# Performance work log

Hardware: AMD Instinct MI355X
Metric: run time of the kernel (lower is better)

Reference implementation:

```python
import jax, jax.numpy as jnp
import numpy as np
import math

D_MODEL = 512
N_HEADS = 8
D_K = D_MODEL // N_HEADS
BS, N_EDGES, N_NODES = 4, 1024, 4096


def setup_inputs() -> dict:
    key = jax.random.key(0)
    ks = jax.random.split(key, 12)
    s = 1.0 / math.sqrt(D_MODEL)
    return {
        "queries": jax.random.normal(ks[0], (BS, N_EDGES, D_MODEL), jnp.float32),
        "keys": jax.random.normal(ks[1], (BS, N_NODES, D_MODEL), jnp.float32),
        "incidence_matrix": jax.random.randint(ks[2], (BS, N_EDGES, N_NODES), 0, 2, jnp.int32),
        "Wq": jax.random.normal(ks[3], (D_MODEL, D_MODEL), jnp.float32) * s,
        "bq": jax.random.normal(ks[4], (D_MODEL,), jnp.float32) * s,
        "Wk": jax.random.normal(ks[5], (D_MODEL, D_MODEL), jnp.float32) * s,
        "bk": jax.random.normal(ks[6], (D_MODEL,), jnp.float32) * s,
        "Wv": jax.random.normal(ks[7], (D_MODEL, D_MODEL), jnp.float32) * s,
        "bv": jax.random.normal(ks[8], (D_MODEL,), jnp.float32) * s,
        "Wo": jax.random.normal(ks[9], (D_MODEL, D_MODEL), jnp.float32) * s,
        "bo": jax.random.normal(ks[10], (D_MODEL,), jnp.float32) * s,
    }


def reference(queries, keys, incidence_matrix, Wq, bq, Wk, bk, Wv, bv, Wo, bo):
    bs, E, _ = queries.shape
    N = keys.shape[1]
    # QKV projections (torch Linear: x @ W.T + b), split heads -> (bs, H, len, d_k)
    Q = (queries @ Wq.T + bq).reshape(bs, E, N_HEADS, D_K).transpose(0, 2, 1, 3)
    K = (keys @ Wk.T + bk).reshape(bs, N, N_HEADS, D_K).transpose(0, 2, 1, 3)
    V = (keys @ Wv.T + bv).reshape(bs, N, N_HEADS, D_K).transpose(0, 2, 1, 3)
    # scores: (bs, H, E, N)
    scores = jnp.einsum("bhed,bhnd->bhen", Q, K) / math.sqrt(D_K)
    mask = (incidence_matrix == 0)[:, None, :, :]  # (bs, 1, E, N)
    scores = jnp.where(mask, jnp.float32(-1e9), scores)
    attn = jax.nn.softmax(scores, axis=-1)
    # dropout is identity in eval mode
    out = jnp.einsum("bhen,bhnd->bhed", attn, V)  # (bs, H, E, d_k)
    out = out.transpose(0, 2, 1, 3).reshape(bs, E, D_MODEL)
    return out @ Wo.T + bo
```

## Files before the change

kernel.cpp:

```cpp
#include <hip/hip_runtime.h>

#define DMODEL 512
#define NHEADS 8
#define DK 64
#define BSZ 4
#define NE 1024
#define NNODE 4096

typedef __attribute__((ext_vector_type(8))) __bf16 bf16x8;
typedef __attribute__((ext_vector_type(4))) float f32x4;
typedef __attribute__((ext_vector_type(8))) unsigned short u16x8;
typedef __attribute__((ext_vector_type(4))) unsigned short u16x4;

static __device__ __forceinline__ unsigned short f2bf(float f) {
    union { float f; unsigned int u; } v; v.f = f;
    unsigned int u = v.u;
    return (unsigned short)((u + 0x7FFFu + ((u >> 16) & 1u)) >> 16);
}

static __device__ __forceinline__ unsigned cvtpk(float lo, float hi) {
    unsigned r;
    asm("v_cvt_pk_bf16_f32 %0, %1, %2" : "=v"(r) : "v"(lo), "v"(hi));
    return r;
}

static __device__ __forceinline__ float exp2v(float x) {
    float r;
    asm("v_exp_f32 %0, %1" : "=v"(r) : "v"(x));
    return r;
}

static __device__ __forceinline__ bf16x8 ldb8(const unsigned short* p) {
    return *reinterpret_cast<const bf16x8*>(p);
}

static __device__ __forceinline__ void gload16(const unsigned short* g,
                                               unsigned short* l) {
    __builtin_amdgcn_global_load_lds(
        (const __attribute__((address_space(1))) unsigned int*)g,
        (__attribute__((address_space(3))) unsigned int*)l, 16, 0, 0);
}

__global__ __launch_bounds__(256) void conv_all(
    const float4* __restrict__ q, const float4* __restrict__ k,
    const float4* __restrict__ wq, const float4* __restrict__ wk,
    const float4* __restrict__ wv, const float4* __restrict__ wo,
    u16x8* __restrict__ qb, u16x8* __restrict__ kb, u16x8* __restrict__ wb) {
    int i = blockIdx.x * 256 + threadIdx.x;
    const float4* s;
    u16x8* d;
    int j;
    if (i < 262144) {
        s = q; d = qb; j = i;
    } else if (i < 1310720) {
        s = k; d = kb; j = i - 262144;
    } else {
        int t = i - 1310720;
        int sel = t >> 15;
        s = sel == 0 ? wq : sel == 1 ? wk : sel == 2 ? wv : wo;
        d = wb + ((size_t)sel << 15);
        j = t & 32767;
    }
    float4 x = s[2 * j];
    float4 y = s[2 * j + 1];
    unsigned u0 = cvtpk(x.x, x.y), u1 = cvtpk(x.z, x.w);
    unsigned u2 = cvtpk(y.x, y.y), u3 = cvtpk(y.z, y.w);
    u16x8 o;
    o[0] = (unsigned short)u0; o[1] = (unsigned short)(u0 >> 16);
    o[2] = (unsigned short)u1; o[3] = (unsigned short)(u1 >> 16);
    o[4] = (unsigned short)u2; o[5] = (unsigned short)(u2 >> 16);
    o[6] = (unsigned short)u3; o[7] = (unsigned short)(u3 >> 16);
    d[j] = o;
}

__global__ __launch_bounds__(256) void maskpack(const int* __restrict__ inc,
                                                unsigned long long* __restrict__ mb) {
    int wid = blockIdx.x * 4 + (threadIdx.x >> 6);
    int lane = threadIdx.x & 63;
#pragma unroll
    for (int j = 0; j < 8; ++j) {
        int g = wid * 8 + j;
        int v = inc[(size_t)g * 64 + lane];
        unsigned long long m = __ballot(v != 0);
        if (lane == 0) mb[g] = m;
    }
}

template <int MODE>
__global__ __launch_bounds__(256) void gemm128(const unsigned short* __restrict__ A,
                                               const unsigned short* __restrict__ W,
                                               const float* __restrict__ bias,
                                               void* __restrict__ Cout, float oscale) {
    int w = threadIdx.x >> 6, l = threadIdx.x & 63;
    int lr = l & 15, lh = l >> 4;
    int wm = w >> 1, wn = w & 1;
    int m0 = blockIdx.x * 128, n0 = blockIdx.y * 128;

    __shared__ unsigned short Ast[2][128][64];
    __shared__ unsigned short Bst[2][128][64];

    int srow = w * 32 + (l >> 3);
    int scu = l & 7;

    auto stage = [&](int bf, int k0) {
#pragma unroll
        for (int ii = 0; ii < 4; ++ii) {
            int row = srow + ii * 8;
            int cu = scu ^ (row & 7);
            gload16(A + (size_t)(m0 + row) * DMODEL + k0 + cu * 8,
                    &Ast[bf][w * 32 + ii * 8][0]);
            gload16(W + (size_t)(n0 + row) * DMODEL + k0 + cu * 8,
                    &Bst[bf][w * 32 + ii * 8][0]);
        }
    };

    f32x4 acc[4][4] = {};

    stage(0, 0);
    __syncthreads();

    int bf = 0;
    for (int t = 0; t < 8; ++t) {
        if (t < 7) stage(bf ^ 1, (t + 1) * 64);
#pragma unroll
        for (int half = 0; half < 2; ++half) {
            bf16x8 af[4], bfr[4];
#pragma unroll
            for (int mf = 0; mf < 4; ++mf)
                af[mf] = ldb8(&Ast[bf][wm * 64 + mf * 16 + lr]
                                  [((half * 4 + lh) ^ (lr & 7)) * 8]);
#pragma unroll
            for (int nf = 0; nf < 4; ++nf)
                bfr[nf] = ldb8(&Bst[bf][wn * 64 + nf * 16 + lr]
                                   [((half * 4 + lh) ^ (lr & 7)) * 8]);
#pragma unroll
            for (int mf = 0; mf < 4; ++mf)
#pragma unroll
                for (int nf = 0; nf < 4; ++nf)
                    acc[mf][nf] = __builtin_amdgcn_mfma_f32_16x16x32_bf16(
                        af[mf], bfr[nf], acc[mf][nf], 0, 0, 0);
        }
        __syncthreads();
        bf ^= 1;
    }

    if constexpr (MODE == 0) {
        unsigned short* C = (unsigned short*)Cout;
#pragma unroll
        for (int nf = 0; nf < 4; ++nf) {
            int ncol = n0 + wn * 64 + nf * 16 + lr;
            float bv = bias[ncol];
#pragma unroll
            for (int mf = 0; mf < 4; ++mf)
#pragma unroll
                for (int r = 0; r < 4; ++r)
                    C[(size_t)(m0 + wm * 64 + mf * 16 + lh * 4 + r) * DMODEL + ncol] =
                        f2bf((acc[mf][nf][r] + bv) * oscale);
        }
    } else if constexpr (MODE == 1) {
        unsigned short* Vt = (unsigned short*)Cout;
        int bb = m0 >> 12;
        int nodebase = (m0 & (NNODE - 1)) + wm * 64;
#pragma unroll
        for (int nf = 0; nf < 4; ++nf) {
            int ncol = n0 + wn * 64 + nf * 16;
            int hh = ncol >> 6;
            int dd = (ncol & 63) + lr;
            float bv = bias[ncol + lr];
#pragma unroll
            for (int mf = 0; mf < 4; ++mf) {
                u16x4 pk;
#pragma unroll
                for (int r = 0; r < 4; ++r) pk[r] = f2bf(acc[mf][nf][r] + bv);
                int node0 = nodebase + mf * 16 + lh * 4;
                *reinterpret_cast<u16x4*>(
                    Vt + (size_t)((bb * NHEADS + hh) * DK + dd) * NNODE + node0) = pk;
            }
        }
    } else {
        float* C = (float*)Cout;
#pragma unroll
        for (int nf = 0; nf < 4; ++nf) {
            int ncol = n0 + wn * 64 + nf * 16 + lr;
            float bv = bias[ncol];
#pragma unroll
            for (int mf = 0; mf < 4; ++mf)
#pragma unroll
                for (int r = 0; r < 4; ++r)
                    C[(size_t)(m0 + wm * 64 + mf * 16 + lh * 4 + r) * DMODEL + ncol] =
                        acc[mf][nf][r] + bv;
        }
    }
}

__global__ __launch_bounds__(256) void attn_kernel(
    const unsigned short* __restrict__ Qb, const unsigned short* __restrict__ Kb,
    const unsigned short* __restrict__ Vt, const unsigned long long* __restrict__ mbits,
    float* __restrict__ Op, float* __restrict__ Lp) {
    int w = threadIdx.x >> 6, l = threadIdx.x & 63;
    int lr = l & 15, lh = l >> 4;
    int id = blockIdx.x;
    int xcd = id & 7, et = (id >> 3) & 15;
    int rest = id >> 7;
    int ps = rest & 3, seg = rest >> 2;
    int pair = xcd * 4 + ps;
    int b = pair >> 3, h = pair & 7;
    int e0 = et * 64 + w * 16;

    __shared__ unsigned short Kst[2][64][64];
    __shared__ unsigned short Vst[2][64][64];
    __shared__ unsigned short Pt[4][16][76];
    unsigned short* Pw = &Pt[w][0][0];

    const unsigned short* Qrow = Qb + (size_t)(b * NE + e0 + lr) * DMODEL + h * DK;
    bf16x8 q0 = ldb8(Qrow + lh * 8);
    bf16x8 q1 = ldb8(Qrow + 32 + lh * 8);

    const unsigned short* Kg =
        Kb + (size_t)(b * NNODE + seg * 2048) * DMODEL + h * DK;
    const unsigned short* Vg =
        Vt + (size_t)((b * NHEADS + h) * DK) * NNODE + seg * 2048;
    const unsigned long long* mrow = mbits + (size_t)(b * NE + e0) * 64 + seg * 32;

    int srow0 = w * 16 + (l >> 3);
    int scol = l & 7;

    f32x4 oacc[4] = {};
    float lsum[4] = {0.f, 0.f, 0.f, 0.f};

    auto stage = [&](int bf, int cb) {
#pragma unroll
        for (int ii = 0; ii < 2; ++ii) {
            int row = srow0 + ii * 8;
            int cu = scol ^ (row & 7);
            gload16(Kg + (size_t)(cb * 64 + row) * DMODEL + cu * 8,
                    &Kst[bf][w * 16 + ii * 8][0]);
            gload16(Vg + (size_t)row * NNODE + cb * 64 + cu * 8,
                    &Vst[bf][w * 16 + ii * 8][0]);
        }
    };

    unsigned long long mcur[4], mnext[4];

    stage(0, 0);
#pragma unroll
    for (int r = 0; r < 4; ++r) mcur[r] = mrow[(lh * 4 + r) * 64];
    __syncthreads();

    int bf = 0;
    for (int cb = 0; cb < 32; ++cb) {
        if (cb < 31) {
            stage(bf ^ 1, cb + 1);
#pragma unroll
            for (int r = 0; r < 4; ++r) mnext[r] = mrow[(lh * 4 + r) * 64 + cb + 1];
        }
        bf16x8 kf[4][2];
#pragma unroll
        for (int t = 0; t < 4; ++t) {
            int row = t * 16 + lr;
            kf[t][0] = ldb8(&Kst[bf][row][((0 + lh) ^ (lr & 7)) * 8]);
            kf[t][1] = ldb8(&Kst[bf][row][((4 + lh) ^ (lr & 7)) * 8]);
        }
        f32x4 s[4] = {};
#pragma unroll
        for (int t = 0; t < 4; ++t) {
            s[t] = __builtin_amdgcn_mfma_f32_16x16x32_bf16(q0, kf[t][0], s[t], 0, 0, 0);
            s[t] = __builtin_amdgcn_mfma_f32_16x16x32_bf16(q1, kf[t][1], s[t], 0, 0, 0);
        }
        bf16x8 vf[2][4];
#pragma unroll
        for (int kk = 0; kk < 2; ++kk)
#pragma unroll
            for (int dt = 0; dt < 4; ++dt) {
                int row = dt * 16 + lr;
                vf[kk][dt] = ldb8(&Vst[bf][row][((kk * 4 + lh) ^ (lr & 7)) * 8]);
            }
#pragma unroll
        for (int t = 0; t < 4; ++t) {
#pragma unroll
            for (int r = 0; r < 4; ++r) {
                float p = exp2v(s[t][r]);
                unsigned half = (t < 2) ? (unsigned)mcur[r] : (unsigned)(mcur[r] >> 32);
                unsigned bits = half >> ((t & 1) * 16 + lr);
                p = (bits & 1u) ? p : 0.0f;
                s[t][r] = p;
                lsum[r] += p;
            }
            unsigned p01 = cvtpk(s[t][0], s[t][1]);
            unsigned p23 = cvtpk(s[t][2], s[t][3]);
            Pw[(lh * 4 + 0) * 76 + t * 16 + lr] = (unsigned short)p01;
            Pw[(lh * 4 + 1) * 76 + t * 16 + lr] = (unsigned short)(p01 >> 16);
            Pw[(lh * 4 + 2) * 76 + t * 16 + lr] = (unsigned short)p23;
            Pw[(lh * 4 + 3) * 76 + t * 16 + lr] = (unsigned short)(p23 >> 16);
        }
#pragma unroll
        for (int kk = 0; kk < 2; ++kk) {
            bf16x8 pa = ldb8(Pw + lr * 76 + kk * 32 + lh * 8);
#pragma unroll
            for (int dt = 0; dt < 4; ++dt) {
                oacc[dt] = __builtin_amdgcn_mfma_f32_16x16x32_bf16(pa, vf[kk][dt],
                                                                   oacc[dt], 0, 0, 0);
            }
        }
        __syncthreads();
        bf ^= 1;
#pragma unroll
        for (int r = 0; r < 4; ++r) mcur[r] = mnext[r];
    }

#pragma unroll
    for (int r = 0; r < 4; ++r) {
        float v = lsum[r];
        v += __shfl_xor(v, 1);
        v += __shfl_xor(v, 2);
        v += __shfl_xor(v, 4);
        v += __shfl_xor(v, 8);
        lsum[r] = v;
    }
    float* Opf = Op + (size_t)seg * (BSZ * NE * DMODEL);
    float* Lpf = Lp + (size_t)seg * (BSZ * NHEADS * NE);
#pragma unroll
    for (int r = 0; r < 4; ++r) {
        size_t row = (size_t)(b * NE + e0 + lh * 4 + r) * DMODEL + h * DK;
#pragma unroll
        for (int dt = 0; dt < 4; ++dt) Opf[row + dt * 16 + lr] = oacc[dt][r];
    }
    if (lr == 0) {
#pragma unroll
        for (int r = 0; r < 4; ++r)
            Lpf[(size_t)(b * NHEADS + h) * NE + e0 + lh * 4 + r] = lsum[r];
    }
}

__global__ __launch_bounds__(256) void combine2(const float* __restrict__ O0,
                                                const float* __restrict__ O1,
                                                const float* __restrict__ L0,
                                                const float* __restrict__ L1,
                                                unsigned short* __restrict__ Ob) {
    int gi = blockIdx.x * 256 + threadIdx.x;
    size_t base = (size_t)gi * 8;
    int row = (int)(base >> 9);
    int h = ((int)base & 511) >> 6;
    int b = row >> 10, e = row & 1023;
    size_t li = (size_t)(b * NHEADS + h) * NE + e;
    float inv = 1.0f / (L0[li] + L1[li]);
    float4 a0 = *reinterpret_cast<const float4*>(O0 + base);
    float4 a1 = *reinterpret_cast<const float4*>(O0 + base + 4);
    float4 b0 = *reinterpret_cast<const float4*>(O1 + base);
    float4 b1 = *reinterpret_cast<const float4*>(O1 + base + 4);
    unsigned u0 = cvtpk((a0.x + b0.x) * inv, (a0.y + b0.y) * inv);
    unsigned u1 = cvtpk((a0.z + b0.z) * inv, (a0.w + b0.w) * inv);
    unsigned u2 = cvtpk((a1.x + b1.x) * inv, (a1.y + b1.y) * inv);
    unsigned u3 = cvtpk((a1.z + b1.z) * inv, (a1.w + b1.w) * inv);
    u16x8 o;
    o[0] = (unsigned short)u0; o[1] = (unsigned short)(u0 >> 16);
    o[2] = (unsigned short)u1; o[3] = (unsigned short)(u1 >> 16);
    o[4] = (unsigned short)u2; o[5] = (unsigned short)(u2 >> 16);
    o[6] = (unsigned short)u3; o[7] = (unsigned short)(u3 >> 16);
    *reinterpret_cast<u16x8*>(Ob + base) = o;
}

extern "C" void kernel_launch(void* const* d_in, const int* in_sizes, int n_in,
                              void* d_out, int out_size, void* d_ws, size_t ws_size,
                              hipStream_t stream) {
    const float* queries = (const float*)d_in[0];
    const float* keys = (const float*)d_in[1];
    const int* inc = (const int*)d_in[2];
    const float* Wq = (const float*)d_in[3];
    const float* bq = (const float*)d_in[4];
    const float* Wk = (const float*)d_in[5];
    const float* bk = (const float*)d_in[6];
    const float* Wv = (const float*)d_in[7];
    const float* bv = (const float*)d_in[8];
    const float* Wo = (const float*)d_in[9];
    const float* bo = (const float*)d_in[10];

    char* base = (char*)d_ws;
    unsigned long long* mbits = (unsigned long long*)base;
    unsigned short* wqb = (unsigned short*)(base + (2u << 20));
    unsigned short* qbf = (unsigned short*)(base + (4u << 20));
    unsigned short* kbf = (unsigned short*)(base + (8u << 20));
    unsigned short* Qb = (unsigned short*)(base + (24u << 20));
    unsigned short* Kb = (unsigned short*)(base + (28u << 20));
    unsigned short* Vt = (unsigned short*)(base + (44u << 20));
    unsigned short* Ob = (unsigned short*)(base + (60u << 20));
    float* Op0 = (float*)(base + (4u << 20));
    float* Lp0 = (float*)(base + (20u << 20));

    conv_all<<<5632, 256, 0, stream>>>((const float4*)queries, (const float4*)keys,
                                       (const float4*)Wq, (const float4*)Wk,
                                       (const float4*)Wv, (const float4*)Wo,
                                       (u16x8*)qbf, (u16x8*)kbf, (u16x8*)wqb);
    maskpack<<<8192, 256, 0, stream>>>(inc, mbits);

    unsigned short* wkb = wqb + DMODEL * DMODEL;
    unsigned short* wvb = wkb + DMODEL * DMODEL;
    unsigned short* wob = wvb + DMODEL * DMODEL;

    gemm128<0><<<dim3(BSZ * NE / 128, 4), 256, 0, stream>>>(qbf, wqb, bq, Qb,
                                                            0.18033688f);
    gemm128<0><<<dim3(BSZ * NNODE / 128, 4), 256, 0, stream>>>(kbf, wkb, bk, Kb, 1.0f);
    gemm128<1><<<dim3(BSZ * NNODE / 128, 4), 256, 0, stream>>>(kbf, wvb, bv, Vt, 1.0f);

    attn_kernel<<<dim3(1024), 256, 0, stream>>>(Qb, Kb, Vt, mbits, Op0, Lp0);

    combine2<<<dim3(1024), 256, 0, stream>>>(Op0, Op0 + (size_t)BSZ * NE * DMODEL, Lp0,
                                             Lp0 + (size_t)BSZ * NHEADS * NE, Ob);

    gemm128<2><<<dim3(BSZ * NE / 128, 4), 256, 0, stream>>>(Ob, wob, bo, d_out, 1.0f);
}
```

Measured before the change: 323.1 us.

## Compute transposed scores per wave so probabilities feed PV MFMA directly

```diff
diff --git a/kernel.cpp b/kernel.cpp
--- a/kernel.cpp
+++ b/kernel.cpp
@@ -11,6 +11,7 @@
 typedef __attribute__((ext_vector_type(4))) float f32x4;
 typedef __attribute__((ext_vector_type(8))) unsigned short u16x8;
 typedef __attribute__((ext_vector_type(4))) unsigned short u16x4;
+typedef __attribute__((ext_vector_type(4))) unsigned int u32x4;
 
 static __device__ __forceinline__ unsigned short f2bf(float f) {
     union { float f; unsigned int u; } v; v.f = f;
@@ -18,15 +19,14 @@
     return (unsigned short)((u + 0x7FFFu + ((u >> 16) & 1u)) >> 16);
 }
 
+static __device__ __forceinline__ float bf2f(unsigned short s) {
+    union { unsigned int u; float f; } v; v.u = ((unsigned int)s) << 16;
+    return v.f;
+}
+
 static __device__ __forceinline__ unsigned cvtpk(float lo, float hi) {
     unsigned r;
     asm("v_cvt_pk_bf16_f32 %0, %1, %2" : "=v"(r) : "v"(lo), "v"(hi));
-    return r;
-}
-
-static __device__ __forceinline__ float exp2v(float x) {
-    float r;
-    asm("v_exp_f32 %0, %1" : "=v"(r) : "v"(x));
     return r;
 }
 
@@ -196,146 +196,140 @@
 __global__ __launch_bounds__(256) void attn_kernel(
     const unsigned short* __restrict__ Qb, const unsigned short* __restrict__ Kb,
     const unsigned short* __restrict__ Vt, const unsigned long long* __restrict__ mbits,
-    float* __restrict__ Op, float* __restrict__ Lp) {
+    unsigned short* __restrict__ Op, float* __restrict__ Lp) {
     int w = threadIdx.x >> 6, l = threadIdx.x & 63;
     int lr = l & 15, lh = l >> 4;
     int id = blockIdx.x;
-    int xcd = id & 7, et = (id >> 3) & 15;
-    int rest = id >> 7;
-    int ps = rest & 3, seg = rest >> 2;
+    int xcd = id & 7, tile = (id >> 3) & 15, ps = id >> 7;
     int pair = xcd * 4 + ps;
     int b = pair >> 3, h = pair & 7;
-    int e0 = et * 64 + w * 16;
+    int e0 = tile * 64;
 
     __shared__ unsigned short Kst[2][64][64];
     __shared__ unsigned short Vst[2][64][64];
-    __shared__ unsigned short Pt[4][16][76];
-    unsigned short* Pw = &Pt[w][0][0];
-
-    const unsigned short* Qrow = Qb + (size_t)(b * NE + e0 + lr) * DMODEL + h * DK;
-    bf16x8 q0 = ldb8(Qrow + lh * 8);
-    bf16x8 q1 = ldb8(Qrow + 32 + lh * 8);
-
-    const unsigned short* Kg =
-        Kb + (size_t)(b * NNODE + seg * 2048) * DMODEL + h * DK;
-    const unsigned short* Vg =
-        Vt + (size_t)((b * NHEADS + h) * DK) * NNODE + seg * 2048;
-    const unsigned long long* mrow = mbits + (size_t)(b * NE + e0) * 64 + seg * 32;
+
+    bf16x8 qf[4][2];
+#pragma unroll
+    for (int et = 0; et < 4; ++et) {
+        const unsigned short* Qrow =
+            Qb + (size_t)(b * NE + e0 + et * 16 + lr) * DMODEL + h * DK;
+        qf[et][0] = ldb8(Qrow + lh * 8);
+        qf[et][1] = ldb8(Qrow + 32 + lh * 8);
+    }
+
+    const unsigned short* Kg = Kb + (size_t)b * NNODE * DMODEL + h * DK;
+    const unsigned short* Vg = Vt + (size_t)((b * NHEADS + h) * DK) * NNODE;
+    const unsigned long long* mbase = mbits + (size_t)(b * NE + e0) * 64;
 
     int srow0 = w * 16 + (l >> 3);
     int scol = l & 7;
 
-    f32x4 oacc[4] = {};
-    float lsum[4] = {0.f, 0.f, 0.f, 0.f};
-
-    auto stage = [&](int bf, int cb) {
+    auto stage = [&](int sb, int cb) {
 #pragma unroll
         for (int ii = 0; ii < 2; ++ii) {
             int row = srow0 + ii * 8;
             int cu = scol ^ (row & 7);
             gload16(Kg + (size_t)(cb * 64 + row) * DMODEL + cu * 8,
-                    &Kst[bf][w * 16 + ii * 8][0]);
+                    &Kst[sb][w * 16 + ii * 8][0]);
             gload16(Vg + (size_t)row * NNODE + cb * 64 + cu * 8,
-                    &Vst[bf][w * 16 + ii * 8][0]);
+                    &Vst[sb][w * 16 + ii * 8][0]);
         }
     };
 
+    f32x4 oacc[4][4] = {};
+    float lsum[4] = {0.f, 0.f, 0.f, 0.f};
+    int shft = w * 16 + lh * 4;
+
     unsigned long long mcur[4], mnext[4];
 
     stage(0, 0);
 #pragma unroll
-    for (int r = 0; r < 4; ++r) mcur[r] = mrow[(lh * 4 + r) * 64];
+    for (int et = 0; et < 4; ++et) mcur[et] = mbase[(size_t)(et * 16 + lr) * 64];
     __syncthreads();
 
     int bf = 0;
-    for (int cb = 0; cb < 32; ++cb) {
-        if (cb < 31) {
+    for (int cb = 0; cb < 64; ++cb) {
+        if (cb < 63) {
             stage(bf ^ 1, cb + 1);
 #pragma unroll
-            for (int r = 0; r < 4; ++r) mnext[r] = mrow[(lh * 4 + r) * 64 + cb + 1];
-        }
-        bf16x8 kf[4][2];
-#pragma unroll
-        for (int t = 0; t < 4; ++t) {
-            int row = t * 16 + lr;
-            kf[t][0] = ldb8(&Kst[bf][row][((0 + lh) ^ (lr & 7)) * 8]);
-            kf[t][1] = ldb8(&Kst[bf][row][((4 + lh) ^ (lr & 7)) * 8]);
-        }
+            for (int et = 0; et < 4; ++et)
+                mnext[et] = mbase[(size_t)(et * 16 + lr) * 64 + cb + 1];
+        }
+        int krow = w * 16 + lr;
+        bf16x8 kf0 = ldb8(&Kst[bf][krow][((0 + lh) ^ (lr & 7)) * 8]);
+        bf16x8 kf1 = ldb8(&Kst[bf][krow][((4 + lh) ^ (lr & 7)) * 8]);
         f32x4 s[4] = {};
 #pragma unroll
-        for (int t = 0; t < 4; ++t) {
-            s[t] = __builtin_amdgcn_mfma_f32_16x16x32_bf16(q0, kf[t][0], s[t], 0, 0, 0);
-            s[t] = __builtin_amdgcn_mfma_f32_16x16x32_bf16(q1, kf[t][1], s[t], 0, 0, 0);
-        }
-        bf16x8 vf[2][4];
-#pragma unroll
-        for (int kk = 0; kk < 2; ++kk)
+        for (int et = 0; et < 4; ++et) {
+            s[et] = __builtin_amdgcn_mfma_f32_16x16x32_bf16(kf0, qf[et][0], s[et], 0, 0, 0);
+            s[et] = __builtin_amdgcn_mfma_f32_16x16x32_bf16(kf1, qf[et][1], s[et], 0, 0, 0);
+        }
+        u32x4 vf[4];
+#pragma unroll
+        for (int dt = 0; dt < 4; ++dt) {
+            int vrow = dt * 16 + lr;
+            int unit = (w * 2 + (lh >> 1)) ^ (lr & 7);
+            const unsigned int* p =
+                (const unsigned int*)(&Vst[bf][vrow][0] + unit * 8 + (lh & 1) * 4);
+            vf[dt][0] = p[0];
+            vf[dt][1] = p[1];
+            vf[dt][2] = 0u;
+            vf[dt][3] = 0u;
+        }
+#pragma unroll
+        for (int et = 0; et < 4; ++et) {
+            unsigned half32 =
+                (shft & 32) ? (unsigned)(mcur[et] >> 32) : (unsigned)mcur[et];
+            unsigned mw = (half32 >> (shft & 31)) & 0xFu;
+            float p0 = (mw & 1u) ? exp2f(s[et][0]) : 0.0f;
+            float p1 = (mw & 2u) ? exp2f(s[et][1]) : 0.0f;
+            float p2 = (mw & 4u) ? exp2f(s[et][2]) : 0.0f;
+            float p3 = (mw & 8u) ? exp2f(s[et][3]) : 0.0f;
+            lsum[et] += (p0 + p1) + (p2 + p3);
+            u32x4 af;
+            af[0] = ((unsigned)f2bf(p1) << 16) | (unsigned)f2bf(p0);
+            af[1] = ((unsigned)f2bf(p3) << 16) | (unsigned)f2bf(p2);
+            af[2] = 0u;
+            af[3] = 0u;
+            bf16x8 a8 = __builtin_bit_cast(bf16x8, af);
 #pragma unroll
             for (int dt = 0; dt < 4; ++dt) {
-                int row = dt * 16 + lr;
-                vf[kk][dt] = ldb8(&Vst[bf][row][((kk * 4 + lh) ^ (lr & 7)) * 8]);
-            }
-#pragma unroll
-        for (int t = 0; t < 4; ++t) {
-#pragma unroll
-            for (int r = 0; r < 4; ++r) {
-                float p = exp2v(s[t][r]);
-                unsigned half = (t < 2) ? (unsigned)mcur[r] : (unsigned)(mcur[r] >> 32);
-                unsigned bits = half >> ((t & 1) * 16 + lr);
-                p = (bits & 1u) ? p : 0.0f;
-                s[t][r] = p;
-                lsum[r] += p;
-            }
-            unsigned p01 = cvtpk(s[t][0], s[t][1]);
-            unsigned p23 = cvtpk(s[t][2], s[t][3]);
-            Pw[(lh * 4 + 0) * 76 + t * 16 + lr] = (unsigned short)p01;
-            Pw[(lh * 4 + 1) * 76 + t * 16 + lr] = (unsigned short)(p01 >> 16);
-            Pw[(lh * 4 + 2) * 76 + t * 16 + lr] = (unsigned short)p23;
-            Pw[(lh * 4 + 3) * 76 + t * 16 + lr] = (unsigned short)(p23 >> 16);
-        }
-#pragma unroll
-        for (int kk = 0; kk < 2; ++kk) {
-            bf16x8 pa = ldb8(Pw + lr * 76 + kk * 32 + lh * 8);
-#pragma unroll
-            for (int dt = 0; dt < 4; ++dt) {
-                oacc[dt] = __builtin_amdgcn_mfma_f32_16x16x32_bf16(pa, vf[kk][dt],
-                                                                   oacc[dt], 0, 0, 0);
+                oacc[et][dt] = __builtin_amdgcn_mfma_f32_16x16x32_bf16(
+                    a8, __builtin_bit_cast(bf16x8, vf[dt]), oacc[et][dt], 0, 0, 0);
             }
         }
         __syncthreads();
         bf ^= 1;
 #pragma unroll
-        for (int r = 0; r < 4; ++r) mcur[r] = mnext[r];
-    }
-
-#pragma unroll
-    for (int r = 0; r < 4; ++r) {
-        float v = lsum[r];
-        v += __shfl_xor(v, 1);
-        v += __shfl_xor(v, 2);
-        v += __shfl_xor(v, 4);
-        v += __shfl_xor(v, 8);
-        lsum[r] = v;
-    }
-    float* Opf = Op + (size_t)seg * (BSZ * NE * DMODEL);
-    float* Lpf = Lp + (size_t)seg * (BSZ * NHEADS * NE);
-#pragma unroll
-    for (int r = 0; r < 4; ++r) {
-        size_t row = (size_t)(b * NE + e0 + lh * 4 + r) * DMODEL + h * DK;
-#pragma unroll
-        for (int dt = 0; dt < 4; ++dt) Opf[row + dt * 16 + lr] = oacc[dt][r];
-    }
-    if (lr == 0) {
-#pragma unroll
-        for (int r = 0; r < 4; ++r)
-            Lpf[(size_t)(b * NHEADS + h) * NE + e0 + lh * 4 + r] = lsum[r];
-    }
-}
-
-__global__ __launch_bounds__(256) void combine2(const float* __restrict__ O0,
-                                                const float* __restrict__ O1,
-                                                const float* __restrict__ L0,
-                                                const float* __restrict__ L1,
+        for (int et = 0; et < 4; ++et) mcur[et] = mnext[et];
+    }
+
+#pragma unroll
+    for (int et = 0; et < 4; ++et) {
+        float v = lsum[et];
+        v += __shfl_xor(v, 16);
+        v += __shfl_xor(v, 32);
+        lsum[et] = v;
+    }
+    unsigned short* Ow = Op + (size_t)w * ((size_t)BSZ * NE * DMODEL);
+#pragma unroll
+    for (int et = 0; et < 4; ++et)
+#pragma unroll
+        for (int dt = 0; dt < 4; ++dt)
+#pragma unroll
+            for (int r = 0; r < 4; ++r)
+                Ow[(size_t)(b * NE + e0 + et * 16 + lh * 4 + r) * DMODEL + h * DK +
+                   dt * 16 + lr] = f2bf(oacc[et][dt][r]);
+    if (lh == 0) {
+        float* Lw = Lp + (size_t)w * ((size_t)BSZ * NHEADS * NE);
+#pragma unroll
+        for (int et = 0; et < 4; ++et)
+            Lw[(size_t)(b * NHEADS + h) * NE + e0 + et * 16 + lr] = lsum[et];
+    }
+}
+
+__global__ __launch_bounds__(256) void combine4(const unsigned short* __restrict__ Op,
+                                                const float* __restrict__ Lp,
                                                 unsigned short* __restrict__ Ob) {
     int gi = blockIdx.x * 256 + threadIdx.x;
     size_t base = (size_t)gi * 8;
@@ -343,15 +337,21 @@
     int h = ((int)base & 511) >> 6;
     int b = row >> 10, e = row & 1023;
     size_t li = (size_t)(b * NHEADS + h) * NE + e;
-    float inv = 1.0f / (L0[li] + L1[li]);
-    float4 a0 = *reinterpret_cast<const float4*>(O0 + base);
-    float4 a1 = *reinterpret_cast<const float4*>(O0 + base + 4);
-    float4 b0 = *reinterpret_cast<const float4*>(O1 + base);
-    float4 b1 = *reinterpret_cast<const float4*>(O1 + base + 4);
-    unsigned u0 = cvtpk((a0.x + b0.x) * inv, (a0.y + b0.y) * inv);
-    unsigned u1 = cvtpk((a0.z + b0.z) * inv, (a0.w + b0.w) * inv);
-    unsigned u2 = cvtpk((a1.x + b1.x) * inv, (a1.y + b1.y) * inv);
-    unsigned u3 = cvtpk((a1.z + b1.z) * inv, (a1.w + b1.w) * inv);
+    const size_t OS = (size_t)BSZ * NE * DMODEL;
+    const size_t LS = (size_t)BSZ * NHEADS * NE;
+    float L = Lp[li] + Lp[LS + li] + Lp[2 * LS + li] + Lp[3 * LS + li];
+    float inv = 1.0f / fmaxf(L, 1e-37f);
+    float acc[8] = {};
+#pragma unroll
+    for (int w2 = 0; w2 < 4; ++w2) {
+        u16x8 v = *reinterpret_cast<const u16x8*>(Op + w2 * OS + base);
+#pragma unroll
+        for (int j = 0; j < 8; ++j) acc[j] += bf2f(v[j]);
+    }
+    unsigned u0 = cvtpk(acc[0] * inv, acc[1] * inv);
+    unsigned u1 = cvtpk(acc[2] * inv, acc[3] * inv);
+    unsigned u2 = cvtpk(acc[4] * inv, acc[5] * inv);
+    unsigned u3 = cvtpk(acc[6] * inv, acc[7] * inv);
     u16x8 o;
     o[0] = (unsigned short)u0; o[1] = (unsigned short)(u0 >> 16);
     o[2] = (unsigned short)u1; o[3] = (unsigned short)(u1 >> 16);
@@ -384,8 +384,8 @@
     unsigned short* Kb = (unsigned short*)(base + (28u << 20));
     unsigned short* Vt = (unsigned short*)(base + (44u << 20));
     unsigned short* Ob = (unsigned short*)(base + (60u << 20));
-    float* Op0 = (float*)(base + (4u << 20));
-    float* Lp0 = (float*)(base + (20u << 20));
+    unsigned short* Opart = (unsigned short*)(base + (4u << 20));
+    float* Lpart = (float*)(base + (20u << 20));
 
     conv_all<<<5632, 256, 0, stream>>>((const float4*)queries, (const float4*)keys,
                                        (const float4*)Wq, (const float4*)Wk,
@@ -402,10 +402,9 @@
     gemm128<0><<<dim3(BSZ * NNODE / 128, 4), 256, 0, stream>>>(kbf, wkb, bk, Kb, 1.0f);
     gemm128<1><<<dim3(BSZ * NNODE / 128, 4), 256, 0, stream>>>(kbf, wvb, bv, Vt, 1.0f);
 
-    attn_kernel<<<dim3(1024), 256, 0, stream>>>(Qb, Kb, Vt, mbits, Op0, Lp0);
-
-    combine2<<<dim3(1024), 256, 0, stream>>>(Op0, Op0 + (size_t)BSZ * NE * DMODEL, Lp0,
-                                             Lp0 + (size_t)BSZ * NHEADS * NE, Ob);
+    attn_kernel<<<dim3(512), 256, 0, stream>>>(Qb, Kb, Vt, mbits, Opart, Lpart);
+
+    combine4<<<dim3(1024), 256, 0, stream>>>(Opart, Lpart, Ob);
 
     gemm128<2><<<dim3(BSZ * NE / 128, 4), 256, 0, stream>>>(Ob, wob, bo, d_out, 1.0f);
 }
```

Result: slower. 341.3 us (+5.6%).
